# Kernel tuning notes

Measured on AMD Instinct MI355X. Metric: run time of the kernel, lower is better.

The kernel has to match this reference:

```python
import jax, jax.numpy as jnp
import numpy as np

N_NODE = 50000
N_EDGE = 800000
NODE_DIM, EDGE_DIM = 3, 4


def _relu(x):
    return jnp.maximum(x, 0)


def setup_inputs() -> dict:
    key = jax.random.key(0)
    ks = jax.random.split(key, 32)
    ki = iter(range(32))

    def w(shape):
        fan = shape[0]
        return (jax.random.normal(ks[next(ki)], shape, jnp.float32) / np.float32(np.sqrt(fan)))

    def b(n):
        return jnp.zeros((n,), jnp.float32)

    inp = {
        'nodes': jax.random.normal(ks[next(ki)], (N_NODE, NODE_DIM), jnp.float32),
        'edges': jax.random.normal(ks[next(ki)], (N_EDGE, EDGE_DIM), jnp.float32),
        'senders': jax.random.randint(ks[next(ki)], (N_EDGE,), 0, N_NODE, jnp.int32),
        'receivers': jax.random.randint(ks[next(ki)], (N_EDGE,), 0, N_NODE, jnp.int32),
        # psi1 encoder: [10 -> 256 -> 256 -> 128], relu after every layer (act_final=True)
        'mw0': w((NODE_DIM * 2 + EDGE_DIM, 256)), 'mb0': b(256),
        'mw1': w((256, 256)), 'mb1': b(256),
        'mw2': w((256, 128)), 'mb2': b(128),
        # psi2 attention: [128 -> 128 -> 128 -> 1], no final act
        'aw0': w((128, 128)), 'ab0': b(128),
        'aw1': w((128, 128)), 'ab1': b(128),
        'aw2': w((128, 1)), 'ab2': b(1),
        # psi3 value: [128 -> 256 -> 128], relu after every layer
        'vw0': w((128, 256)), 'vb0': b(256),
        'vw1': w((256, 128)), 'vb1': b(128),
        # psi4 decoder: [128 -> 256 -> 256 -> 1], no final act
        'uw0': w((128, 256)), 'ub0': b(256),
        'uw1': w((256, 256)), 'ub1': b(256),
        'uw2': w((256, 1)), 'ub2': b(1),
    }
    return inp


def reference(nodes, edges, senders, receivers,
              mw0, mb0, mw1, mb1, mw2, mb2,
              aw0, ab0, aw1, ab1, aw2, ab2,
              vw0, vb0, vw1, vb1,
              uw0, ub0, uw1, ub1, uw2, ub2):
    n_node = nodes.shape[0]
    # gather endpoint features and concat with edge features: (E, 2*node_dim+edge_dim)
    z = jnp.concatenate([nodes[senders], nodes[receivers], edges], axis=-1)
    # psi1 encoder (act_final=True)
    q = _relu(_relu(_relu(z @ mw0 + mb0) @ mw1 + mb1) @ mw2 + mb2)  # (E,128)
    # psi2 attention logits (no final act)
    w = (_relu(_relu(q @ aw0 + ab0) @ aw1 + ab1) @ aw2 + ab2)[:, 0]  # (E,)
    # segment softmax over receivers (matches torch scatter_reduce amax with -1e9 init)
    m = jax.ops.segment_max(w, receivers, num_segments=n_node)
    m = jnp.maximum(m, jnp.float32(-1e9))
    ex = jnp.exp(w - m[receivers])
    s = jax.ops.segment_sum(ex, receivers, num_segments=n_node)
    attn = ex / (s[receivers] + 1e-12)  # (E,)
    # psi3 value (act_final=True)
    v = _relu(_relu(q @ vw0 + vb0) @ vw1 + vb1)  # (E,128)
    # attention-weighted scatter-add aggregation to receiver nodes
    aggr = jax.ops.segment_sum(attn[:, None] * v, receivers, num_segments=n_node)  # (N,128)
    # psi4 decoder (no final act)
    out = _relu(_relu(aggr @ uw0 + ub0) @ uw1 + ub1) @ uw2 + ub2  # (N,1)
    return out
```

## Files before the change

### kernel.cpp

```cpp
#include <hip/hip_runtime.h>
#include <stdint.h>

#define NN_NODE 50000
#define NN_EDGE 800000

typedef _Float16 f16;
typedef _Float16 f16x2 __attribute__((ext_vector_type(2)));
typedef _Float16 f16x4 __attribute__((ext_vector_type(4)));
typedef _Float16 f16x8 __attribute__((ext_vector_type(8)));
typedef float f32x4 __attribute__((ext_vector_type(4)));

#define WT_MW0   0
#define WT_MW1   8192
#define WT_MW2   73728
#define WT_AW0   106496
#define WT_AW1   122880
#define WT_VW0   139264
#define WT_VW1   172032
#define WT_UW0   204800
#define WT_UW1   237568
#define WT_TOTAL 303104

#define V_OFF      606208ull
#define WL_OFF     205406208ull
#define CNT_OFF    208606208ull
#define BASE_OFF   208806208ull
#define AGGR_OFF   209006208ull

__device__ __forceinline__ int swz(int row, int col) {
    return row * 256 + ((((col >> 3) ^ (row & 7))) << 3) + (col & 7);
}

template<int K, int N>
__device__ __forceinline__ void mfma_layer(const f16* in, int inoff,
        const f16* __restrict__ wt, const float* __restrict__ bias,
        f16* out, int outoff, int tid)
{
    const int wave = tid >> 6;
    const int lane = tid & 63;
    const int l15  = lane & 15;
    const int quad = lane >> 4;
    constexpr int NCT = N >> 4;
    constexpr int NKS = K >> 5;

    f16x8 af[4][NKS];
#pragma unroll
    for (int ms = 0; ms < 4; ++ms)
#pragma unroll
        for (int ks = 0; ks < NKS; ++ks)
            af[ms][ks] = *(const f16x8*)(in + swz(ms * 16 + l15, inoff + ks * 32 + quad * 8));

#pragma unroll 1
    for (int ct = wave; ct < NCT; ct += 4) {
        f16x8 bf[NKS];
        const f16* wrow = wt + (size_t)(ct * 16 + l15) * K + quad * 8;
#pragma unroll
        for (int ks = 0; ks < NKS; ++ks) bf[ks] = *(const f16x8*)(wrow + ks * 32);
        const int f0 = ct * 16 + quad * 4;
        const float4 bv = *(const float4*)(bias + f0);
#pragma unroll
        for (int ms = 0; ms < 4; ++ms) {
            f32x4 acc = {0.f, 0.f, 0.f, 0.f};
#pragma unroll
            for (int ks = 0; ks < NKS; ++ks)
                acc = __builtin_amdgcn_mfma_f32_16x16x32_f16(bf[ks], af[ms][ks], acc, 0, 0, 0);
            f16x4 o;
            o[0] = (f16)fmaxf(acc[0] + bv.x, 0.f);
            o[1] = (f16)fmaxf(acc[1] + bv.y, 0.f);
            o[2] = (f16)fmaxf(acc[2] + bv.z, 0.f);
            o[3] = (f16)fmaxf(acc[3] + bv.w, 0.f);
            *(f16x4*)(out + swz(ms * 16 + l15, outoff + f0)) = o;
        }
    }
}

struct WSeg { const float* src; int K, N, Kpad, dstOff; };
struct WSegs { WSeg s[9]; };

__global__ void prep_kernel(WSegs segs, f16* __restrict__ wt) {
    int idx = blockIdx.x * 256 + threadIdx.x;
    if (idx >= WT_TOTAL) return;
    int off = idx;
#pragma unroll
    for (int i = 0; i < 9; ++i) {
        int sz = segs.s[i].N * segs.s[i].Kpad;
        if (off < sz) {
            int n = off / segs.s[i].Kpad;
            int k = off - n * segs.s[i].Kpad;
            f16 val = (f16)0.f;
            if (k < segs.s[i].K) val = (f16)segs.s[i].src[k * segs.s[i].N + n];
            wt[segs.s[i].dstOff + off] = val;
            return;
        }
        off -= sz;
    }
}

__global__ void hist_kernel(const int* __restrict__ receivers, int* __restrict__ cnt) {
    int e = blockIdx.x * 256 + threadIdx.x;
    atomicAdd(&cnt[receivers[e]], 1);
}

__global__ __launch_bounds__(1024) void scan_kernel(int* __restrict__ cnt, int* __restrict__ base) {
    __shared__ int psum[1024];
    const int tid = threadIdx.x;
    const int CH = (NN_NODE + 1023) / 1024;
    const int lo = tid * CH;
    const int hi = min(lo + CH, NN_NODE);
    int s = 0;
    for (int i = lo; i < hi; ++i) s += cnt[i];
    psum[tid] = s;
    __syncthreads();
    for (int d = 1; d < 1024; d <<= 1) {
        int v = (tid >= d) ? psum[tid - d] : 0;
        __syncthreads();
        psum[tid] += v;
        __syncthreads();
    }
    int run = psum[tid] - s;
    for (int i = lo; i < hi; ++i) {
        int c = cnt[i];
        base[i] = run;
        cnt[i] = run;
        run += c;
    }
}

__global__ __launch_bounds__(256, 2) void edge_kernel(
        const float* __restrict__ nodes, const float* __restrict__ edges,
        const int* __restrict__ senders, const int* __restrict__ receivers,
        const f16* __restrict__ wt,
        const float* __restrict__ mb0, const float* __restrict__ mb1, const float* __restrict__ mb2,
        const float* __restrict__ ab0, const float* __restrict__ ab1,
        const float* __restrict__ aw2, const float* __restrict__ ab2,
        const float* __restrict__ vb0, const float* __restrict__ vb1,
        f16* __restrict__ vout, float* __restrict__ wlog, int* __restrict__ cursor)
{
    __shared__ f16 ldsbuf[2 * 64 * 256];
    __shared__ int spos[64];
    f16* bufA = ldsbuf;
    f16* bufB = ldsbuf + 64 * 256;
    const int tid = threadIdx.x;
    const int e0 = blockIdx.x * 64;

    {
        int e = tid & 63, part = tid >> 6;
        if (part == 0) {
            int s = senders[e0 + e];
            for (int c = 0; c < 3; ++c) bufA[swz(e, c)] = (f16)nodes[s * 3 + c];
        } else if (part == 1) {
            int r = receivers[e0 + e];
            for (int c = 0; c < 3; ++c) bufA[swz(e, 3 + c)] = (f16)nodes[r * 3 + c];
        } else if (part == 2) {
            const float4 ev = *(const float4*)(edges + (size_t)(e0 + e) * 4);
            bufA[swz(e, 6)] = (f16)ev.x; bufA[swz(e, 7)] = (f16)ev.y;
            bufA[swz(e, 8)] = (f16)ev.z; bufA[swz(e, 9)] = (f16)ev.w;
        } else {
            for (int c = 10; c < 32; ++c) bufA[swz(e, c)] = (f16)0.f;
        }
    }
    __syncthreads();

    mfma_layer< 32, 256>(bufA, 0, wt + WT_MW0, mb0, bufB, 0, tid); __syncthreads();
    mfma_layer<256, 256>(bufB, 0, wt + WT_MW1, mb1, bufA, 0, tid); __syncthreads();
    mfma_layer<256, 128>(bufA, 0, wt + WT_MW2, mb2, bufB, 0, tid); __syncthreads();
    mfma_layer<128, 128>(bufB, 0, wt + WT_AW0, ab0, bufA, 0, tid); __syncthreads();
    mfma_layer<128, 128>(bufA, 0, wt + WT_AW1, ab1, bufA, 128, tid); __syncthreads();

    {
        int e = tid >> 2, part = tid & 3;
        float sum = 0.f;
        for (int c = part * 32; c < part * 32 + 32; ++c)
            sum += (float)bufA[swz(e, 128 + c)] * aw2[c];
        sum += __shfl_down(sum, 2);
        sum += __shfl_down(sum, 1);
        if (part == 0) {
            float wv = sum + ab2[0];
            int r = receivers[e0 + e];
            int pos = atomicAdd(&cursor[r], 1);
            spos[e] = pos;
            wlog[pos] = wv;
        }
    }
    __syncthreads();

    mfma_layer<128, 256>(bufB, 0, wt + WT_VW0, vb0, bufA, 0, tid); __syncthreads();
    mfma_layer<256, 128>(bufA, 0, wt + WT_VW1, vb1, bufB, 0, tid); __syncthreads();

    {
        int row = tid >> 2, j = tid & 3;
        uint4* dst = (uint4*)(vout + (size_t)spos[row] * 128);
#pragma unroll
        for (int i = 0; i < 4; ++i) {
            int chunk = j * 4 + i;
            const uint4 val = *(const uint4*)(bufB + row * 256 + ((chunk ^ (row & 7)) * 8));
            dst[chunk] = val;
        }
    }
}

__global__ __launch_bounds__(256) void aggregate_kernel(
        const float* __restrict__ wlog, const f16* __restrict__ v,
        const int* __restrict__ base, float* __restrict__ aggr)
{
    const int tid = threadIdx.x;
    const int n = blockIdx.x * 4 + (tid >> 6);
    const int lane = tid & 63;
    const int st = base[n];
    const int en = (n == NN_NODE - 1) ? NN_EDGE : base[n + 1];

    float mx = -1e9f;
    for (int i = st + lane; i < en; i += 64) mx = fmaxf(mx, wlog[i]);
#pragma unroll
    for (int d = 1; d < 64; d <<= 1) mx = fmaxf(mx, __shfl_xor(mx, d));

    float sm = 0.f;
    for (int i = st + lane; i < en; i += 64) sm += __expf(wlog[i] - mx);
#pragma unroll
    for (int d = 1; d < 64; d <<= 1) sm += __shfl_xor(sm, d);
    const float inv = 1.f / (sm + 1e-12f);

    float acc0 = 0.f, acc1 = 0.f;
    const f16* vp = v + (size_t)st * 128 + lane * 2;
    for (int i = st; i < en; ++i, vp += 128) {
        float attn = __expf(wlog[i] - mx) * inv;
        f16x2 vv = *(const f16x2*)vp;
        acc0 += attn * (float)vv[0];
        acc1 += attn * (float)vv[1];
    }
    float2 o; o.x = acc0; o.y = acc1;
    *(float2*)(aggr + (size_t)n * 128 + lane * 2) = o;
}

__global__ __launch_bounds__(256, 2) void node_kernel(
        const float* __restrict__ aggr, const f16* __restrict__ wt,
        const float* __restrict__ ub0, const float* __restrict__ ub1,
        const float* __restrict__ uw2, const float* __restrict__ ub2,
        float* __restrict__ out)
{
    __shared__ f16 ldsbuf[2 * 64 * 256];
    f16* bufA = ldsbuf;
    f16* bufB = ldsbuf + 64 * 256;
    const int tid = threadIdx.x;
    const int n0 = blockIdx.x * 64;
    {
        int row = tid >> 2, j = tid & 3;
        int n = n0 + row;
        if (n < NN_NODE) {
            const float4* src = (const float4*)(aggr + (size_t)n * 128 + j * 32);
#pragma unroll
            for (int i = 0; i < 8; ++i) {
                float4 t4 = src[i];
                int c = j * 32 + i * 4;
                bufA[swz(row, c + 0)] = (f16)t4.x;
                bufA[swz(row, c + 1)] = (f16)t4.y;
                bufA[swz(row, c + 2)] = (f16)t4.z;
                bufA[swz(row, c + 3)] = (f16)t4.w;
            }
        } else {
#pragma unroll
            for (int i = 0; i < 32; ++i) bufA[swz(row, j * 32 + i)] = (f16)0.f;
        }
    }
    __syncthreads();
    mfma_layer<128, 256>(bufA, 0, wt + WT_UW0, ub0, bufB, 0, tid); __syncthreads();
    mfma_layer<256, 256>(bufB, 0, wt + WT_UW1, ub1, bufA, 0, tid); __syncthreads();
    {
        int e = tid >> 2, part = tid & 3;
        float sum = 0.f;
        for (int c = part * 64; c < part * 64 + 64; ++c)
            sum += (float)bufA[swz(e, c)] * uw2[c];
        sum += __shfl_down(sum, 2);
        sum += __shfl_down(sum, 1);
        int n = n0 + e;
        if (part == 0 && n < NN_NODE) out[n] = sum + ub2[0];
    }
}

extern "C" void kernel_launch(void* const* d_in, const int* in_sizes, int n_in,
                              void* d_out, int out_size, void* d_ws, size_t ws_size,
                              hipStream_t stream)
{
    const float* nodes     = (const float*)d_in[0];
    const float* edges     = (const float*)d_in[1];
    const int*   senders   = (const int*)d_in[2];
    const int*   receivers = (const int*)d_in[3];
    const float* mw0 = (const float*)d_in[4];  const float* mb0 = (const float*)d_in[5];
    const float* mw1 = (const float*)d_in[6];  const float* mb1 = (const float*)d_in[7];
    const float* mw2 = (const float*)d_in[8];  const float* mb2 = (const float*)d_in[9];
    const float* aw0 = (const float*)d_in[10]; const float* ab0 = (const float*)d_in[11];
    const float* aw1 = (const float*)d_in[12]; const float* ab1 = (const float*)d_in[13];
    const float* aw2 = (const float*)d_in[14]; const float* ab2 = (const float*)d_in[15];
    const float* vw0 = (const float*)d_in[16]; const float* vb0 = (const float*)d_in[17];
    const float* vw1 = (const float*)d_in[18]; const float* vb1 = (const float*)d_in[19];
    const float* uw0 = (const float*)d_in[20]; const float* ub0 = (const float*)d_in[21];
    const float* uw1 = (const float*)d_in[22]; const float* ub1 = (const float*)d_in[23];
    const float* uw2 = (const float*)d_in[24]; const float* ub2 = (const float*)d_in[25];

    char* ws = (char*)d_ws;
    f16*   wt   = (f16*)ws;
    f16*   vbuf = (f16*)(ws + V_OFF);
    float* wlog = (float*)(ws + WL_OFF);
    int*   cnt  = (int*)(ws + CNT_OFF);
    int*   base = (int*)(ws + BASE_OFF);
    float* aggr = (float*)(ws + AGGR_OFF);
    float* out  = (float*)d_out;

    hipMemsetAsync(cnt, 0, NN_NODE * sizeof(int), stream);

    WSegs segs = {{
        { mw0,  10, 256,  32, WT_MW0 },
        { mw1, 256, 256, 256, WT_MW1 },
        { mw2, 256, 128, 256, WT_MW2 },
        { aw0, 128, 128, 128, WT_AW0 },
        { aw1, 128, 128, 128, WT_AW1 },
        { vw0, 128, 256, 128, WT_VW0 },
        { vw1, 256, 128, 256, WT_VW1 },
        { uw0, 128, 256, 128, WT_UW0 },
        { uw1, 256, 256, 256, WT_UW1 },
    }};
    prep_kernel<<<(WT_TOTAL + 255) / 256, 256, 0, stream>>>(segs, wt);

    hist_kernel<<<NN_EDGE / 256, 256, 0, stream>>>(receivers, cnt);
    scan_kernel<<<1, 1024, 0, stream>>>(cnt, base);

    edge_kernel<<<NN_EDGE / 64, 256, 0, stream>>>(nodes, edges, senders, receivers, wt,
        mb0, mb1, mb2, ab0, ab1, aw2, ab2, vb0, vb1, vbuf, wlog, cnt);

    aggregate_kernel<<<NN_NODE / 4, 256, 0, stream>>>(wlog, vbuf, base, aggr);

    node_kernel<<<(NN_NODE + 63) / 64, 256, 0, stream>>>(aggr, wt, ub0, ub1, uw2, ub2, out);
}
```

Baseline: 1.073 ms.

## Prefetch next-layer weights across layers and fuse attention/value epilogues

Rewrites the edge kernel's MLP chain so each layer's weight fragments are double-buffered in registers: the next column tile and the first tile of the following layer are loaded while the current MFMAs run. The attention output projection is folded into the aw1 layer epilogue as a per-wave partial dot product reduced through a small LDS array. The final value layer writes straight to the sorted global positions, which removes an LDS round trip, a barrier and one sync. Input staging now uses vectorized 16-byte LDS writes. The extra live register arrays (bfA/bfB, double buffers) increase VGPR pressure under launch_bounds(256,2) and may cause spills.

```diff
diff --git a/kernel.cpp b/kernel.cpp
--- a/kernel.cpp
+++ b/kernel.cpp
@@ -31,8 +31,104 @@
     return row * 256 + ((((col >> 3) ^ (row & 7))) << 3) + (col & 7);
 }
 
+template<int K, int N, int NKN, int EPI>
+__device__ __forceinline__ void mlayer(const f16* in, int inoff,
+        const f16* __restrict__ wt, const float* __restrict__ bias,
+        f16* out, int outoff,
+        f16x8* bf0, const f16* __restrict__ wtn, f16x8* bfn,
+        const float* __restrict__ aw2, float* lpart,
+        f16* __restrict__ vout, const int* sposp, int tid)
+{
+    const int wave = tid >> 6;
+    const int lane = tid & 63;
+    const int l15  = lane & 15;
+    const int quad = lane >> 4;
+    constexpr int NKS = K >> 5;
+    constexpr int NCT = N >> 4;
+    constexpr int ITC = NCT / 4;
+
+    f16x8 af[4][NKS];
+#pragma unroll
+    for (int ms = 0; ms < 4; ++ms)
+#pragma unroll
+        for (int ks = 0; ks < NKS; ++ks)
+            af[ms][ks] = *(const f16x8*)(in + swz(ms * 16 + l15, inoff + ks * 32 + quad * 8));
+
+    if constexpr (NKN > 0) {
+        const f16* wrow = wtn + (size_t)(wave * 16 + l15) * (NKN * 32) + quad * 8;
+#pragma unroll
+        for (int ks = 0; ks < NKN; ++ks) bfn[ks] = *(const f16x8*)(wrow + ks * 32);
+    }
+
+    int   sposv[4];
+    float preg[4];
+    if constexpr (EPI == 2) {
+#pragma unroll
+        for (int ms = 0; ms < 4; ++ms) sposv[ms] = sposp[ms * 16 + l15];
+    }
+    if constexpr (EPI == 1) {
+#pragma unroll
+        for (int ms = 0; ms < 4; ++ms) preg[ms] = 0.f;
+    }
+
+    f16x8 bfl[2][NKS > 0 ? NKS : 1];
+#pragma unroll
+    for (int ks = 0; ks < NKS; ++ks) bfl[0][ks] = bf0[ks];
+
+#pragma unroll
+    for (int i = 0; i < ITC; ++i) {
+        const int ct = wave + i * 4;
+        if (i + 1 < ITC) {
+            const f16* wrow = wt + (size_t)((ct + 4) * 16 + l15) * K + quad * 8;
+#pragma unroll
+            for (int ks = 0; ks < NKS; ++ks)
+                bfl[(i + 1) & 1][ks] = *(const f16x8*)(wrow + ks * 32);
+        }
+        const int f0 = ct * 16 + quad * 4;
+        const float4 bv = *(const float4*)(bias + f0);
+        float4 awv;
+        if constexpr (EPI == 1) awv = *(const float4*)(aw2 + f0);
+#pragma unroll
+        for (int ms = 0; ms < 4; ++ms) {
+            f32x4 acc = {0.f, 0.f, 0.f, 0.f};
+#pragma unroll
+            for (int ks = 0; ks < NKS; ++ks)
+                acc = __builtin_amdgcn_mfma_f32_16x16x32_f16(bfl[i & 1][ks], af[ms][ks], acc, 0, 0, 0);
+            if constexpr (EPI == 0) {
+                f16x4 o;
+                o[0] = (f16)fmaxf(acc[0] + bv.x, 0.f);
+                o[1] = (f16)fmaxf(acc[1] + bv.y, 0.f);
+                o[2] = (f16)fmaxf(acc[2] + bv.z, 0.f);
+                o[3] = (f16)fmaxf(acc[3] + bv.w, 0.f);
+                *(f16x4*)(out + swz(ms * 16 + l15, outoff + f0)) = o;
+            } else if constexpr (EPI == 1) {
+                preg[ms] += fmaxf(acc[0] + bv.x, 0.f) * awv.x
+                          + fmaxf(acc[1] + bv.y, 0.f) * awv.y
+                          + fmaxf(acc[2] + bv.z, 0.f) * awv.z
+                          + fmaxf(acc[3] + bv.w, 0.f) * awv.w;
+            } else {
+                f16x4 o;
+                o[0] = (f16)fmaxf(acc[0] + bv.x, 0.f);
+                o[1] = (f16)fmaxf(acc[1] + bv.y, 0.f);
+                o[2] = (f16)fmaxf(acc[2] + bv.z, 0.f);
+                o[3] = (f16)fmaxf(acc[3] + bv.w, 0.f);
+                *(f16x4*)(vout + (size_t)sposv[ms] * 128 + f0) = o;
+            }
+        }
+    }
+    if constexpr (EPI == 1) {
+#pragma unroll
+        for (int ms = 0; ms < 4; ++ms) {
+            float r = preg[ms];
+            r += __shfl_xor(r, 16);
+            r += __shfl_xor(r, 32);
+            if (quad == 0) lpart[wave * 64 + ms * 16 + l15] = r;
+        }
+    }
+}
+
 template<int K, int N>
-__device__ __forceinline__ void mfma_layer(const f16* in, int inoff,
+__device__ __forceinline__ void mfma_layer_basic(const f16* in, int inoff,
         const f16* __restrict__ wt, const float* __restrict__ bias,
         f16* out, int outoff, int tid)
 {
@@ -42,14 +138,12 @@
     const int quad = lane >> 4;
     constexpr int NCT = N >> 4;
     constexpr int NKS = K >> 5;
-
     f16x8 af[4][NKS];
 #pragma unroll
     for (int ms = 0; ms < 4; ++ms)
 #pragma unroll
         for (int ks = 0; ks < NKS; ++ks)
             af[ms][ks] = *(const f16x8*)(in + swz(ms * 16 + l15, inoff + ks * 32 + quad * 8));
-
 #pragma unroll 1
     for (int ct = wave; ct < NCT; ct += 4) {
         f16x8 bf[NKS];
@@ -138,65 +232,69 @@
 {
     __shared__ f16 ldsbuf[2 * 64 * 256];
     __shared__ int spos[64];
+    __shared__ float lpart[256];
     f16* bufA = ldsbuf;
     f16* bufB = ldsbuf + 64 * 256;
     const int tid = threadIdx.x;
     const int e0 = blockIdx.x * 64;
+    const int wave = tid >> 6;
+    const int lane = tid & 63;
+    const int l15  = lane & 15;
+    const int quad = lane >> 4;
+
+    f16x8 bfA[8], bfB[8];
 
     {
-        int e = tid & 63, part = tid >> 6;
-        if (part == 0) {
+        const f16* wrow = wt + WT_MW0 + (size_t)(wave * 16 + l15) * 32 + quad * 8;
+        bfA[0] = *(const f16x8*)wrow;
+    }
+
+    {
+        const int e = tid & 63, c = tid >> 6;
+        f16x8 zv = {(f16)0.f,(f16)0.f,(f16)0.f,(f16)0.f,(f16)0.f,(f16)0.f,(f16)0.f,(f16)0.f};
+        if (c == 0) {
             int s = senders[e0 + e];
-            for (int c = 0; c < 3; ++c) bufA[swz(e, c)] = (f16)nodes[s * 3 + c];
-        } else if (part == 1) {
             int r = receivers[e0 + e];
-            for (int c = 0; c < 3; ++c) bufA[swz(e, 3 + c)] = (f16)nodes[r * 3 + c];
-        } else if (part == 2) {
-            const float4 ev = *(const float4*)(edges + (size_t)(e0 + e) * 4);
-            bufA[swz(e, 6)] = (f16)ev.x; bufA[swz(e, 7)] = (f16)ev.y;
-            bufA[swz(e, 8)] = (f16)ev.z; bufA[swz(e, 9)] = (f16)ev.w;
-        } else {
-            for (int c = 10; c < 32; ++c) bufA[swz(e, c)] = (f16)0.f;
-        }
-    }
-    __syncthreads();
-
-    mfma_layer< 32, 256>(bufA, 0, wt + WT_MW0, mb0, bufB, 0, tid); __syncthreads();
-    mfma_layer<256, 256>(bufB, 0, wt + WT_MW1, mb1, bufA, 0, tid); __syncthreads();
-    mfma_layer<256, 128>(bufA, 0, wt + WT_MW2, mb2, bufB, 0, tid); __syncthreads();
-    mfma_layer<128, 128>(bufB, 0, wt + WT_AW0, ab0, bufA, 0, tid); __syncthreads();
-    mfma_layer<128, 128>(bufA, 0, wt + WT_AW1, ab1, bufA, 128, tid); __syncthreads();
-
-    {
-        int e = tid >> 2, part = tid & 3;
-        float sum = 0.f;
-        for (int c = part * 32; c < part * 32 + 32; ++c)
-            sum += (float)bufA[swz(e, 128 + c)] * aw2[c];
-        sum += __shfl_down(sum, 2);
-        sum += __shfl_down(sum, 1);
-        if (part == 0) {
-            float wv = sum + ab2[0];
-            int r = receivers[e0 + e];
-            int pos = atomicAdd(&cursor[r], 1);
-            spos[e] = pos;
-            wlog[pos] = wv;
-        }
-    }
-    __syncthreads();
-
-    mfma_layer<128, 256>(bufB, 0, wt + WT_VW0, vb0, bufA, 0, tid); __syncthreads();
-    mfma_layer<256, 128>(bufA, 0, wt + WT_VW1, vb1, bufB, 0, tid); __syncthreads();
-
-    {
-        int row = tid >> 2, j = tid & 3;
-        uint4* dst = (uint4*)(vout + (size_t)spos[row] * 128);
-#pragma unroll
-        for (int i = 0; i < 4; ++i) {
-            int chunk = j * 4 + i;
-            const uint4 val = *(const uint4*)(bufB + row * 256 + ((chunk ^ (row & 7)) * 8));
-            dst[chunk] = val;
-        }
-    }
+            const float2 ev = *(const float2*)(edges + (size_t)(e0 + e) * 4);
+            zv[0] = (f16)nodes[s * 3 + 0]; zv[1] = (f16)nodes[s * 3 + 1]; zv[2] = (f16)nodes[s * 3 + 2];
+            zv[3] = (f16)nodes[r * 3 + 0]; zv[4] = (f16)nodes[r * 3 + 1]; zv[5] = (f16)nodes[r * 3 + 2];
+            zv[6] = (f16)ev.x; zv[7] = (f16)ev.y;
+        } else if (c == 1) {
+            const float2 ev = *(const float2*)(edges + (size_t)(e0 + e) * 4 + 2);
+            zv[0] = (f16)ev.x; zv[1] = (f16)ev.y;
+        }
+        *(f16x8*)(bufA + e * 256 + ((c ^ (e & 7)) << 3)) = zv;
+    }
+    __syncthreads();
+
+    mlayer< 32, 256, 8, 0>(bufA, 0, wt + WT_MW0, mb0, bufB, 0, bfA, wt + WT_MW1, bfB,
+                           nullptr, nullptr, nullptr, nullptr, tid);
+    __syncthreads();
+    mlayer<256, 256, 8, 0>(bufB, 0, wt + WT_MW1, mb1, bufA, 0, bfB, wt + WT_MW2, bfA,
+                           nullptr, nullptr, nullptr, nullptr, tid);
+    __syncthreads();
+    mlayer<256, 128, 4, 0>(bufA, 0, wt + WT_MW2, mb2, bufB, 0, bfA, wt + WT_AW0, bfB,
+                           nullptr, nullptr, nullptr, nullptr, tid);
+    __syncthreads();
+    mlayer<128, 128, 4, 0>(bufB, 0, wt + WT_AW0, ab0, bufA, 0, bfB, wt + WT_AW1, bfA,
+                           nullptr, nullptr, nullptr, nullptr, tid);
+    __syncthreads();
+    mlayer<128, 128, 4, 1>(bufA, 0, wt + WT_AW1, ab1, nullptr, 0, bfA, wt + WT_VW0, bfB,
+                           aw2, lpart, nullptr, nullptr, tid);
+    __syncthreads();
+
+    if (tid < 64) {
+        float wv = lpart[tid] + lpart[64 + tid] + lpart[128 + tid] + lpart[192 + tid] + ab2[0];
+        int r = receivers[e0 + tid];
+        int pos = atomicAdd(&cursor[r], 1);
+        spos[tid] = pos;
+        wlog[pos] = wv;
+    }
+    mlayer<128, 256, 8, 0>(bufB, 0, wt + WT_VW0, vb0, bufA, 0, bfB, wt + WT_VW1, bfA,
+                           nullptr, nullptr, nullptr, nullptr, tid);
+    __syncthreads();
+    mlayer<256, 128, 0, 2>(bufA, 0, wt + WT_VW1, vb1, nullptr, 0, bfA, nullptr, nullptr,
+                           nullptr, nullptr, vout, spos, tid);
 }
 
 __global__ __launch_bounds__(256) void aggregate_kernel(
@@ -263,8 +361,8 @@
         }
     }
     __syncthreads();
-    mfma_layer<128, 256>(bufA, 0, wt + WT_UW0, ub0, bufB, 0, tid); __syncthreads();
-    mfma_layer<256, 256>(bufB, 0, wt + WT_UW1, ub1, bufA, 0, tid); __syncthreads();
+    mfma_layer_basic<128, 256>(bufA, 0, wt + WT_UW0, ub0, bufB, 0, tid); __syncthreads();
+    mfma_layer_basic<256, 256>(bufB, 0, wt + WT_UW1, ub1, bufA, 0, tid); __syncthreads();
     {
         int e = tid >> 2, part = tid & 3;
         float sum = 0.f;
```

Result: faster. 995.7 us (-7.2%).
